# Kernel optimization log

Measured on AMD Instinct MI355X. Metric: run time of the kernel, lower is better.

## Reference

```python
import jax, jax.numpy as jnp
import numpy as np

L, B, S, D, H, F = 4, 8, 512, 512, 8, 2048
KS = (1, 3, 5)
DEPTH = D // H


def causal_conv(x, W, b):
    # x: [B,S,D], W: [k,D,D] (WIO), causal left pad k-1
    k = W.shape[0]
    y = jax.lax.conv_general_dilated(x, W, (1,), [(k - 1, 0)],
                                     dimension_numbers=('NWC', 'WIO', 'NWC'))
    return y + b


def layer_norm(x, g, b, eps=1e-6):
    mu = jnp.mean(x, -1, keepdims=True)
    var = jnp.mean((x - mu) ** 2, -1, keepdims=True)
    return (x - mu) * jax.lax.rsqrt(var + eps) * g + b


def split_heads(t):
    return t.reshape(B, S, H, DEPTH).transpose(0, 2, 1, 3)  # [B,H,S,depth]


def setup_inputs() -> dict:
    key = jax.random.key(0)
    keys = iter(jax.random.split(key, 16))
    rn = lambda shape, s=0.02: jax.random.normal(next(keys), shape, jnp.float32) * s
    inp = {"x": jax.random.normal(next(keys), (B, S, D), jnp.float32)}
    for k in KS:
        inp[f"Wq{k}"] = rn((L, k, D, D))
        inp[f"Wk{k}"] = rn((L, k, D, D))
    inp["bq"] = jnp.zeros((L, 3, D), jnp.float32)
    inp["bk"] = jnp.zeros((L, 3, D), jnp.float32)
    inp["Wv"] = rn((L, 3, 1, D, D))
    inp["bv"] = jnp.zeros((L, 3, D), jnp.float32)
    inp["Wo"] = rn((L, D, D)); inp["bo"] = jnp.zeros((L, D), jnp.float32)
    inp["W1"] = rn((L, D, F)); inp["b1"] = jnp.zeros((L, F), jnp.float32)
    inp["W2"] = rn((L, F, D)); inp["b2"] = jnp.zeros((L, D), jnp.float32)
    inp["ln1_g"] = jnp.ones((L, D), jnp.float32); inp["ln1_b"] = jnp.zeros((L, D), jnp.float32)
    inp["ln2_g"] = jnp.ones((L, D), jnp.float32); inp["ln2_b"] = jnp.zeros((L, D), jnp.float32)
    return inp


def reference(x, Wq1, Wq3, Wq5, Wk1, Wk3, Wk5, bq, bk, Wv, bv, Wo, bo,
              W1, b1, W2, b2, ln1_g, ln1_b, ln2_g, ln2_b):
    # causal look-ahead mask: 1 - band_part(ones, -1, 0), added as mask * -1e9
    neg_mask = (1.0 - jnp.tril(jnp.ones((S, S), jnp.float32))) * -1e9
    scale = 1.0 / jnp.sqrt(jnp.float32(DEPTH))
    Wqs, Wks = (Wq1, Wq3, Wq5), (Wk1, Wk3, Wk5)
    for l in range(L):
        outs = []
        for i in range(len(KS)):
            q = split_heads(causal_conv(x, Wqs[i][l], bq[l, i]))
            k = split_heads(causal_conv(x, Wks[i][l], bk[l, i]))
            v = split_heads(causal_conv(x, Wv[l, i], bv[l, i]))
            logits = jnp.einsum('bhqd,bhkd->bhqk', q, k) * scale + neg_mask
            a = jax.nn.softmax(logits, axis=-1)
            o = jnp.einsum('bhqk,bhkd->bhqd', a, v)
            outs.append(o.transpose(0, 2, 1, 3).reshape(B, S, D))
        attn_out = ((outs[0] + outs[1] + outs[2]) / 3.0) @ Wo[l] + bo[l]
        out1 = layer_norm(attn_out + x, ln1_g[l], ln1_b[l])
        ffn = jax.nn.relu(out1 @ W1[l] + b1[l]) @ W2[l] + b2[l]
        x = layer_norm(ffn + out1, ln2_g[l], ln2_b[l])
    return x
```

## Files before the change

### kernel.cpp

```cpp
#include <hip/hip_runtime.h>
#include <cstdint>
#include <cstddef>

#define Dm 512
#define Sm 512
#define Bm 8
#define Hm 8
#define Fm 2048
#define Mm 4096
#define Lm 4

typedef __bf16 bf16x8 __attribute__((ext_vector_type(8)));
typedef float  fx4    __attribute__((ext_vector_type(4)));
typedef float  fx2    __attribute__((ext_vector_type(2)));
typedef unsigned short u16;
typedef unsigned short u16x4 __attribute__((ext_vector_type(4)));
typedef short s16x8 __attribute__((ext_vector_type(8)));

__device__ __forceinline__ u16 f2b(float f) {
  union { float f; uint32_t u; } v; v.f = f;
  uint32_t u = v.u;
  return (u16)((u + 0x7fffu + ((u >> 16) & 1u)) >> 16);
}
__device__ __forceinline__ float b2f(u16 h) {
  union { uint32_t u; float f; } v; v.u = ((uint32_t)h) << 16;
  return v.f;
}

__device__ __forceinline__ void gload16(const void* g, void* l) {
  __builtin_amdgcn_global_load_lds(
      (const __attribute__((address_space(1))) void*)g,
      (__attribute__((address_space(3))) void*)l, 16, 0, 0);
}

template<int N>
__device__ __forceinline__ void vwait() {
  if constexpr (N == 4)      asm volatile("s_waitcnt vmcnt(4)" ::: "memory");
  else if constexpr (N == 8) asm volatile("s_waitcnt vmcnt(8)" ::: "memory");
  else                       asm volatile("s_waitcnt vmcnt(0)" ::: "memory");
}

__global__ void cast_bf16_kernel(const float* __restrict__ in, u16* __restrict__ out,
                                 u16* __restrict__ zpad) {
  int i = (blockIdx.x * 256 + threadIdx.x) * 4;
  fx4 v = *(const fx4*)(in + i);
  u16x4 o;
  #pragma unroll
  for (int j = 0; j < 4; ++j) o[j] = f2b(v[j]);
  *(u16x4*)(out + i) = o;
  if (blockIdx.x == 0) { zpad[threadIdx.x] = 0; zpad[threadIdx.x + 256] = 0; }
}

__global__ void avg3_kernel(const u16* __restrict__ o3, u16* __restrict__ out) {
  int i = (blockIdx.x * 256 + threadIdx.x) * 4;
  u16x4 a = *(const u16x4*)(o3 + i);
  u16x4 b = *(const u16x4*)(o3 + (size_t)Mm*Dm + i);
  u16x4 c = *(const u16x4*)(o3 + (size_t)2*Mm*Dm + i);
  u16x4 r;
  #pragma unroll
  for (int j = 0; j < 4; ++j)
    r[j] = f2b((b2f(a[j]) + b2f(b[j]) + b2f(c[j])) * (1.f/3.f));
  *(u16x4*)(out + i) = r;
}

__global__ void ln_kernel(const float* __restrict__ in, const float* __restrict__ gam,
                          const float* __restrict__ bet, float* __restrict__ outf,
                          u16* __restrict__ outb) {
  int row = blockIdx.x;
  int t = threadIdx.x;
  const float* x = in + (size_t)row * Dm;
  fx4 v0 = *(const fx4*)(x + t*4);
  fx4 v1 = *(const fx4*)(x + 256 + t*4);
  float s = 0.f, sq = 0.f;
  #pragma unroll
  for (int j = 0; j < 4; ++j) { s += v0[j] + v1[j]; sq += v0[j]*v0[j] + v1[j]*v1[j]; }
  #pragma unroll
  for (int off = 1; off < 64; off <<= 1) { s += __shfl_xor(s, off, 64); sq += __shfl_xor(sq, off, 64); }
  float mu  = s * (1.f/Dm);
  float var = sq * (1.f/Dm) - mu*mu;
  float rstd = rsqrtf(var + 1e-6f);
  fx4 g0 = *(const fx4*)(gam + t*4), g1 = *(const fx4*)(gam + 256 + t*4);
  fx4 b0 = *(const fx4*)(bet + t*4), b1 = *(const fx4*)(bet + 256 + t*4);
  float* of = outf + (size_t)row*Dm;
  u16*   ob = outb + (size_t)row*Dm;
  fx4 y0, y1; u16x4 h0, h1;
  #pragma unroll
  for (int j = 0; j < 4; ++j) {
    y0[j] = (v0[j]-mu)*rstd*g0[j] + b0[j];
    y1[j] = (v1[j]-mu)*rstd*g1[j] + b1[j];
    h0[j] = f2b(y0[j]); h1[j] = f2b(y1[j]);
  }
  *(fx4*)(of + t*4) = y0; *(fx4*)(of + 256 + t*4) = y1;
  *(u16x4*)(ob + t*4) = h0; *(u16x4*)(ob + 256 + t*4) = h1;
}

#define TST 130
__global__ void prep_kernel(u16* __restrict__ packed,
    const float* __restrict__ Wq1, const float* __restrict__ Wq3, const float* __restrict__ Wq5,
    const float* __restrict__ Wk1, const float* __restrict__ Wk3, const float* __restrict__ Wk5,
    const float* __restrict__ Wv,  const float* __restrict__ Wo,
    const float* __restrict__ W1,  const float* __restrict__ W2, int layer) {
  __shared__ float T[64 * TST];
  constexpr int t0[13] = {0,32,128,288,320,416,576,608,640,672,704,832,960};
  int bid = blockIdx.x;
  int seg = 0;
  while (bid >= t0[seg+1]) ++seg;
  int local = bid - t0[seg];
  const float* src; int K, N;
  switch (seg) {
    case 0:  src = Wq1 + (size_t)layer*512*512;   K = 512;  N = 512;  break;
    case 1:  src = Wq3 + (size_t)layer*3*512*512; K = 1536; N = 512;  break;
    case 2:  src = Wq5 + (size_t)layer*5*512*512; K = 2560; N = 512;  break;
    case 3:  src = Wk1 + (size_t)layer*512*512;   K = 512;  N = 512;  break;
    case 4:  src = Wk3 + (size_t)layer*3*512*512; K = 1536; N = 512;  break;
    case 5:  src = Wk5 + (size_t)layer*5*512*512; K = 2560; N = 512;  break;
    case 6:  src = Wv + (size_t)(layer*3+0)*512*512; K = 512; N = 512; break;
    case 7:  src = Wv + (size_t)(layer*3+1)*512*512; K = 512; N = 512; break;
    case 8:  src = Wv + (size_t)(layer*3+2)*512*512; K = 512; N = 512; break;
    case 9:  src = Wo + (size_t)layer*512*512;    K = 512;  N = 512;  break;
    case 10: src = W1 + (size_t)layer*512*2048;   K = 512;  N = 2048; break;
    default: src = W2 + (size_t)layer*2048*512;   K = 2048; N = 512;  break;
  }
  int KT = K >> 6;
  int ntile = local / KT, ktile = local - ntile*KT;
  const float* sb = src + (size_t)(ktile*64)*N + ntile*128;
  int tid = threadIdx.x;
  #pragma unroll
  for (int i = 0; i < 16; ++i) {
    int idx = i*256 + tid;
    int row = idx >> 6, col2 = (idx & 63) * 2;
    fx2 v = *(const fx2*)(sb + (size_t)row*N + col2);
    *(fx2*)(&T[row*TST + col2]) = v;
  }
  __syncthreads();
  u16* dst = packed + ((size_t)bid << 13);
  #pragma unroll
  for (int j = 0; j < 4; ++j) {
    int z = j*256 + tid;
    int row = z >> 3;
    int c = (z & 7) ^ (row & 7);
    s16x8 o;
    #pragma unroll
    for (int e = 0; e < 8; ++e) o[e] = (short)f2b(T[(c*8 + e)*TST + row]);
    *(s16x8*)(dst + z*8) = o;
  }
}

#define GEMM_STEP(IDX, CB, NB, BC, BN, NRv, NW)                                   \
  {                                                                              \
    bool hn = (IDX) + 1 < ntiles;                                                \
    if (hn) {                                                                    \
      stageA(NB);                                                                \
      ++skt; if (skt == KTt) { skt = 0; ++st; }                                  \
      const u16* wtn = WtN + ((size_t)((IDX) + 1) << 13);                        \
      _Pragma("unroll")                                                          \
      for (int kk = 0; kk < 2; ++kk)                                             \
        _Pragma("unroll")                                                        \
        for (int n = 0; n < NRv; ++n) {                                          \
          int row = wn*(NRv*16) + n*16 + r16;                                    \
          BN[kk][n] = *(const bf16x8*)(wtn + (row << 6) + (((kk*4 + g) ^ (row & 7)) << 3)); \
        }                                                                        \
    }                                                                            \
    bf16x8 a_[2][4];                                                             \
    _Pragma("unroll")                                                            \
    for (int kk = 0; kk < 2; ++kk)                                               \
      _Pragma("unroll")                                                          \
      for (int m = 0; m < 4; ++m) {                                              \
        int row = wm*64 + m*16 + r16;                                            \
        a_[kk][m] = *(const bf16x8*)(&As[CB][(row << 6) + (((kk*4 + g) ^ (row & 7)) << 3)]); \
      }                                                                          \
    __builtin_amdgcn_s_setprio(1);                                               \
    _Pragma("unroll")                                                            \
    for (int kk = 0; kk < 2; ++kk)                                               \
      _Pragma("unroll")                                                          \
      for (int m = 0; m < 4; ++m)                                                \
        _Pragma("unroll")                                                        \
        for (int n = 0; n < NRv; ++n)                                            \
          acc[m][n] = __builtin_amdgcn_mfma_f32_16x16x32_bf16(a_[kk][m], BC[kk][n], acc[m][n], 0, 0, 0); \
    __builtin_amdgcn_s_setprio(0);                                               \
    vwait<2*NRv>();                                                              \
    __builtin_amdgcn_s_barrier();                                                \
  }

__global__ __launch_bounds__(256, 2) void conv_all(const u16* __restrict__ xb,
    const u16* __restrict__ packed,
    const float* __restrict__ bq, const float* __restrict__ bk, const float* __restrict__ bv,
    u16* __restrict__ qb, u16* __restrict__ kb, u16* __restrict__ vT, int layer,
    const u16* __restrict__ zpad) {
  __shared__ __align__(16) u16 As[2][8192];
  constexpr int t0c[9]   = {0,32,128,288,320,416,576,608,640};
  constexpr int tapsc[9] = {1,3,5,1,3,5,1,1,1};
  constexpr int order[9] = {2,5,1,4,0,3,6,7,8};
  int bid = blockIdx.x;
  int unit = order[bid >> 7];
  int local = bid & 127;
  int mtile = local >> 2, ntile = local & 3;
  int taps = tapsc[unit];
  int brow = mtile * 128, bcol = ntile * 128;
  int tid = threadIdx.x, lane = tid & 63, wid = tid >> 6;
  int wm = wid >> 1, wn = wid & 1;
  int r16 = lane & 15, g = lane >> 4;
  const u16* WtN = packed + ((size_t)(t0c[unit] + ntile * taps * 8) << 13);
  fx4 acc[4][4] = {};
  int ntiles = taps * 8;
  const int KTt = 8;
  int st = 0, skt = 0;
  auto stageA = [&](int bufi) {
    int shift = taps - 1 - st;
    int c0 = skt << 6;
    #pragma unroll
    for (int j = 0; j < 4; ++j) {
      int zb = wid*256 + j*64;
      int zz = zb + lane;
      int row = zz >> 3, c = (zz & 7) ^ (row & 7);
      int s = (brow + row) & (Sm - 1);
      const u16* src = (s >= shift) ? (xb + (size_t)(brow + row - shift)*Dm + c0 + c*8) : zpad;
      gload16(src, &As[bufi][zb * 8]);
    }
  };
  bf16x8 bA[2][4], bB[2][4];
  stageA(0);
  ++skt; if (skt == KTt) { skt = 0; ++st; }
  #pragma unroll
  for (int kk = 0; kk < 2; ++kk)
    #pragma unroll
    for (int n = 0; n < 4; ++n) {
      int row = wn*64 + n*16 + r16;
      bA[kk][n] = *(const bf16x8*)(WtN + (row << 6) + (((kk*4 + g) ^ (row & 7)) << 3));
    }
  __syncthreads();
  for (int base = 0; base < ntiles; base += 2) {
    GEMM_STEP(base,     0, 1, bA, bB, 4, 2)
    GEMM_STEP(base + 1, 1, 0, bB, bA, 4, 2)
  }
  const float* bias; u16* outp;
  if (unit < 3)      { bias = bq + (size_t)(layer*3 + unit)*Dm;   outp = qb + (size_t)unit*Mm*Dm; }
  else if (unit < 6) { bias = bk + (size_t)(layer*3 + unit-3)*Dm; outp = kb + (size_t)(unit-3)*Mm*Dm; }
  else               { bias = bv + (size_t)(layer*3 + unit-6)*Dm; outp = vT + ((size_t)(unit-6) << 21); }
  if (unit < 6) {
    #pragma unroll
    for (int m = 0; m < 4; ++m) {
      int row0 = brow + wm*64 + m*16 + g*4;
      #pragma unroll
      for (int n = 0; n < 4; ++n) {
        int col = bcol + wn*64 + n*16 + r16;
        float bv_ = bias[col];
        #pragma unroll
        for (int r = 0; r < 4; ++r)
          outp[(size_t)(row0 + r)*Dm + col] = f2b(acc[m][n][r] + bv_);
      }
    }
  } else {
    #pragma unroll
    for (int m = 0; m < 4; ++m) {
      int row0 = brow + wm*64 + m*16 + g*4;
      int bidx = row0 >> 9, spos = row0 & 511;
      #pragma unroll
      for (int n = 0; n < 4; ++n) {
        int col = bcol + wn*64 + n*16 + r16;
        int hh = col >> 6, dd = col & 63;
        float bv_ = bias[col];
        u16x4 pk;
        #pragma unroll
        for (int r = 0; r < 4; ++r) pk[r] = f2b(acc[m][n][r] + bv_);
        *(u16x4*)(outp + (((size_t)(bidx*8 + hh)*64 + dd) << 9) + spos) = pk;
      }
    }
  }
}

template<int MODE, int BMt, int WN, bool CAUSAL>
__device__ __forceinline__ void gemm_core(const u16* __restrict__ A, int lda, int Ktap, int taps,
    const u16* __restrict__ Wt, const float* __restrict__ bias, const float* __restrict__ res,
    u16* __restrict__ outb, float* __restrict__ outf, int N, const u16* __restrict__ zpad) {
  constexpr int NR = 128 / (16 * WN);
  constexpr int AD = BMt / 32;
  __shared__ __align__(16) u16 As[2][BMt * 64];
  int tid = threadIdx.x, lane = tid & 63, wid = tid >> 6;
  int wm = (WN == 2) ? (wid >> 1) : 0;
  int wn = (WN == 2) ? (wid & 1) : wid;
  int r16 = lane & 15, g = lane >> 4;
  int brow = blockIdx.x * BMt, bcol = blockIdx.y * 128;
  const int KTt = Ktap >> 6;
  const u16* WtN = Wt + ((size_t)(blockIdx.y * taps * KTt) << 13);
  fx4 acc[4][NR] = {};
  int ntiles = taps * KTt;
  int st = 0, skt = 0;
  auto stageA = [&](int bufi) {
    int shift = taps - 1 - st;
    int c0 = skt << 6;
    #pragma unroll
    for (int j = 0; j < AD; ++j) {
      int zb = wid*(BMt*2) + j*64;
      int zz = zb + lane;
      int row = zz >> 3, c = (zz & 7) ^ (row & 7);
      const u16* src;
      if (CAUSAL) {
        int s = (brow + row) & (Sm - 1);
        src = (s >= shift) ? (A + (size_t)(brow + row - shift)*lda + c0 + c*8) : zpad;
      } else {
        src = A + (size_t)(brow + row)*lda + c0 + c*8;
      }
      gload16(src, &As[bufi][zb * 8]);
    }
  };
  bf16x8 bA[2][NR], bB[2][NR];
  stageA(0);
  ++skt; if (skt == KTt) { skt = 0; ++st; }
  #pragma unroll
  for (int kk = 0; kk < 2; ++kk)
    #pragma unroll
    for (int n = 0; n < NR; ++n) {
      int row = wn*(NR*16) + n*16 + r16;
      bA[kk][n] = *(const bf16x8*)(WtN + (row << 6) + (((kk*4 + g) ^ (row & 7)) << 3));
    }
  __syncthreads();
  for (int base = 0; base < ntiles; base += 2) {
    GEMM_STEP(base,     0, 1, bA, bB, NR, WN)
    GEMM_STEP(base + 1, 1, 0, bB, bA, NR, WN)
  }
  #pragma unroll
  for (int m = 0; m < 4; ++m) {
    int row0 = brow + wm*64 + m*16 + g*4;
    #pragma unroll
    for (int n = 0; n < NR; ++n) {
      int col = bcol + wn*(NR*16) + n*16 + r16;
      float bv_ = bias[col];
      #pragma unroll
      for (int r = 0; r < 4; ++r) {
        size_t idx = (size_t)(row0 + r)*N + col;
        float v = acc[m][n][r] + bv_;
        if (MODE == 0)      outb[idx] = f2b(v);
        else if (MODE == 1) outb[idx] = f2b(fmaxf(v, 0.f));
        else                outf[idx] = v + res[idx];
      }
    }
  }
}

template<int MODE, int BMt, int WN, int LB>
__global__ __launch_bounds__(256, LB) void gemm_dense(const u16* __restrict__ A, int lda, int K,
    const u16* __restrict__ Wt, const float* __restrict__ bias, const float* __restrict__ res,
    u16* __restrict__ outb, float* __restrict__ outf, int N) {
  gemm_core<MODE, BMt, WN, false>(A, lda, K, 1, Wt, bias, res, outb, outf, N, nullptr);
}

__global__ __launch_bounds__(256, 3) void attn_kernel(const u16* __restrict__ qb,
    const u16* __restrict__ kb, const u16* __restrict__ vTb, u16* __restrict__ ob) {
  __shared__ __align__(16) u16 Ks[2][4096];
  __shared__ __align__(16) u16 Vs[2][4096];
  __shared__ __align__(16) u16 Ps[4][1024];
  int a = blockIdx.x, bh = blockIdx.y, br = blockIdx.z;
  int b = bh >> 3, h = bh & 7;
  const u16* q  = qb + (size_t)br*Mm*Dm;
  const u16* k  = kb + (size_t)br*Mm*Dm;
  const u16* vT = vTb + (((size_t)br << 21) + ((size_t)bh << 15));
  u16* o = ob + (size_t)br*Mm*Dm;
  int tid = threadIdx.x, lane = tid & 63, wid = tid >> 6;
  int r16 = lane & 15, g = lane >> 4;
  size_t rowbase = (size_t)b * Sm;
  int qt[2] = {7 - a, a};
  int nkt = qt[0] + 1;

  bf16x8 qa[2][2];
  #pragma unroll
  for (int t2 = 0; t2 < 2; ++t2)
    #pragma unroll
    for (int c = 0; c < 2; ++c)
      qa[t2][c] = *(const bf16x8*)(q + (rowbase + qt[t2]*64 + wid*16 + r16)*Dm + h*64 + c*32 + g*8);

  float m_[2][4], l_[2][4];
  fx4 accO[2][4] = {};
  #pragma unroll
  for (int t2 = 0; t2 < 2; ++t2)
    #pragma unroll
    for (int r = 0; r < 4; ++r) { m_[t2][r] = -3.0e38f; l_[t2][r] = 0.f; }

  auto stage = [&](int kt, int bufi) {
    #pragma unroll
    for (int it = 0; it < 2; ++it) {
      int zb = wid*128 + it*64;
      int zz = zb + lane;
      int row = zz >> 3, c = (zz & 7) ^ (row & 7);
      gload16(k + (rowbase + kt*64 + row)*Dm + h*64 + c*8, &Ks[bufi][zb * 8]);
      gload16(vT + ((size_t)row << 9) + kt*64 + c*8, &Vs[bufi][zb * 8]);
    }
  };
  stage(0, 0);
  __syncthreads();

  for (int kt = 0; kt < nkt; ++kt) {
    int cur = kt & 1;
    if (kt + 1 < nkt) stage(kt + 1, cur ^ 1);
    #pragma unroll
    for (int t2 = 0; t2 < 2; ++t2) {
      if (t2 == 0 || kt <= qt[1]) {
        fx4 sacc[4] = {};
        #pragma unroll
        for (int c = 0; c < 2; ++c)
          #pragma unroll
          for (int n = 0; n < 4; ++n) {
            int row = n*16 + r16;
            bf16x8 kf = *(const bf16x8*)(&Ks[cur][(row << 6) + (((c*4 + g) ^ (row & 7)) << 3)]);
            sacc[n] = __builtin_amdgcn_mfma_f32_16x16x32_bf16(qa[t2][c], kf, sacc[n], 0, 0, 0);
          }
        float sv[4][4];
        bool diag = (kt == qt[t2]);
        #pragma unroll
        for (int n = 0; n < 4; ++n)
          #pragma unroll
          for (int r = 0; r < 4; ++r) {
            float s = sacc[n][r] * 0.125f;
            if (diag && (n*16 + r16 > wid*16 + g*4 + r)) s = -3.0e38f;
            sv[n][r] = s;
          }
        #pragma unroll
        for (int r = 0; r < 4; ++r) {
          float rm = fmaxf(fmaxf(sv[0][r], sv[1][r]), fmaxf(sv[2][r], sv[3][r]));
          #pragma unroll
          for (int off = 1; off < 16; off <<= 1) rm = fmaxf(rm, __shfl_xor(rm, off, 64));
          float mnew = fmaxf(m_[t2][r], rm);
          float corr = __expf(m_[t2][r] - mnew);
          m_[t2][r] = mnew;
          float rs = 0.f;
          #pragma unroll
          for (int n = 0; n < 4; ++n) { float p = __expf(sv[n][r] - mnew); sv[n][r] = p; rs += p; }
          #pragma unroll
          for (int off = 1; off < 16; off <<= 1) rs += __shfl_xor(rs, off, 64);
          l_[t2][r] = l_[t2][r]*corr + rs;
          #pragma unroll
          for (int n = 0; n < 4; ++n) accO[t2][n][r] *= corr;
        }
        #pragma unroll
        for (int n = 0; n < 4; ++n)
          #pragma unroll
          for (int r = 0; r < 4; ++r) {
            int qq = g*4 + r;
            Ps[wid][(qq << 6) + (((n*2 + (r16 >> 3)) ^ (qq & 7)) << 3) + (r16 & 7)] = f2b(sv[n][r]);
          }
        #pragma unroll
        for (int kk = 0; kk < 2; ++kk) {
          bf16x8 pa = *(const bf16x8*)(&Ps[wid][(r16 << 6) + (((kk*4 + g) ^ (r16 & 7)) << 3)]);
          #pragma unroll
          for (int n = 0; n < 4; ++n) {
            int row = n*16 + r16;
            bf16x8 vf = *(const bf16x8*)(&Vs[cur][(row << 6) + (((kk*4 + g) ^ (row & 7)) << 3)]);
            accO[t2][n] = __builtin_amdgcn_mfma_f32_16x16x32_bf16(pa, vf, accO[t2][n], 0, 0, 0);
          }
        }
      }
    }
    __syncthreads();
  }
  #pragma unroll
  for (int t2 = 0; t2 < 2; ++t2)
    #pragma unroll
    for (int n = 0; n < 4; ++n)
      #pragma unroll
      for (int r = 0; r < 4; ++r) {
        int qrow = qt[t2]*64 + wid*16 + g*4 + r;
        o[(rowbase + qrow)*Dm + h*64 + n*16 + r16] = f2b(accO[t2][n][r] / l_[t2][r]);
      }
}

extern "C" void kernel_launch(void* const* d_in, const int* in_sizes, int n_in,
                              void* d_out, int out_size, void* d_ws, size_t ws_size,
                              hipStream_t stream) {
  const float* x_in = (const float*)d_in[0];
  const float* Wq1 = (const float*)d_in[1];
  const float* Wk1 = (const float*)d_in[2];
  const float* Wq3 = (const float*)d_in[3];
  const float* Wk3 = (const float*)d_in[4];
  const float* Wq5 = (const float*)d_in[5];
  const float* Wk5 = (const float*)d_in[6];
  const float* bq  = (const float*)d_in[7];
  const float* bk  = (const float*)d_in[8];
  const float* Wv  = (const float*)d_in[9];
  const float* bv  = (const float*)d_in[10];
  const float* Wo  = (const float*)d_in[11];
  const float* bo  = (const float*)d_in[12];
  const float* W1  = (const float*)d_in[13];
  const float* b1  = (const float*)d_in[14];
  const float* W2  = (const float*)d_in[15];
  const float* b2  = (const float*)d_in[16];
  const float* ln1g = (const float*)d_in[17];
  const float* ln1b = (const float*)d_in[18];
  const float* ln2g = (const float*)d_in[19];
  const float* ln2b = (const float*)d_in[20];

  char* ws = (char*)d_ws;
  size_t off = 0;
  auto alloc = [&](size_t bytes) { void* p = ws + off; off += (bytes + 255) & ~(size_t)255; return p; };
  float* x_f32 = (float*)alloc((size_t)Mm*Dm*4);
  u16*   xb    = (u16*)  alloc((size_t)Mm*Dm*2);
  u16*   qbuf  = (u16*)  alloc((size_t)3*Mm*Dm*2);
  u16*   kbuf  = (u16*)  alloc((size_t)3*Mm*Dm*2);
  u16*   vT    = (u16*)  alloc((size_t)3*Mm*Dm*2);
  u16*   obuf  = (u16*)  alloc((size_t)3*Mm*Dm*2);
  u16*   avgb  = (u16*)  alloc((size_t)Mm*Dm*2);
  float* pre   = (float*)alloc((size_t)Mm*Dm*4);
  float* out1f = (float*)alloc((size_t)Mm*Dm*4);
  u16*   out1b = (u16*)  alloc((size_t)Mm*Dm*2);
  u16*   midb  = (u16*)  alloc((size_t)Mm*Fm*2);
  u16*   packed= (u16*)  alloc((size_t)960*8192*2);
  u16*   zpad  = (u16*)  alloc(1024);

  cast_bf16_kernel<<<2048, 256, 0, stream>>>(x_in, xb, zpad);
  for (int l = 0; l < Lm; ++l) {
    const float* xs = (l == 0) ? x_in : x_f32;
    prep_kernel<<<960, 256, 0, stream>>>(packed, Wq1, Wq3, Wq5, Wk1, Wk3, Wk5,
                                         Wv, Wo, W1, W2, l);
    conv_all<<<1152, 256, 0, stream>>>(
        xb, packed, bq, bk, bv, qbuf, kbuf, vT, l, zpad);
    attn_kernel<<<dim3(4, 64, 3), 256, 0, stream>>>(qbuf, kbuf, vT, obuf);
    avg3_kernel<<<2048, 256, 0, stream>>>(obuf, avgb);
    gemm_dense<2, 64, 4, 3><<<dim3(64, 4), 256, 0, stream>>>(
        avgb, 512, 512, packed + ((size_t)672 << 13), bo + (size_t)l*Dm, xs, nullptr, pre, 512);
    ln_kernel<<<4096, 64, 0, stream>>>(pre, ln1g + (size_t)l*Dm, ln1b + (size_t)l*Dm, out1f, out1b);
    gemm_dense<1, 128, 2, 2><<<dim3(32, 16), 256, 0, stream>>>(
        out1b, 512, 512, packed + ((size_t)704 << 13), b1 + (size_t)l*Fm, nullptr, midb, nullptr, 2048);
    gemm_dense<2, 64, 4, 3><<<dim3(64, 4), 256, 0, stream>>>(
        midb, 2048, 2048, packed + ((size_t)832 << 13), b2 + (size_t)l*Dm, out1f, nullptr, pre, 512);
    float* lnout = (l == Lm-1) ? (float*)d_out : x_f32;
    ln_kernel<<<4096, 64, 0, stream>>>(pre, ln2g + (size_t)l*Dm, ln2b + (size_t)l*Dm, lnout, xb);
  }
}
```

Baseline: 620.4 us.

## Restructure GEMM main loop with per-half-K waits and full-width warp tiles

```diff
diff --git a/kernel.cpp b/kernel.cpp
--- a/kernel.cpp
+++ b/kernel.cpp
@@ -35,9 +35,10 @@
 
 template<int N>
 __device__ __forceinline__ void vwait() {
-  if constexpr (N == 4)      asm volatile("s_waitcnt vmcnt(4)" ::: "memory");
-  else if constexpr (N == 8) asm volatile("s_waitcnt vmcnt(8)" ::: "memory");
-  else                       asm volatile("s_waitcnt vmcnt(0)" ::: "memory");
+  if constexpr (N == 8)       asm volatile("s_waitcnt vmcnt(8)"  ::: "memory");
+  else if constexpr (N == 12) asm volatile("s_waitcnt vmcnt(12)" ::: "memory");
+  else if constexpr (N == 20) asm volatile("s_waitcnt vmcnt(20)" ::: "memory");
+  else                        asm volatile("s_waitcnt vmcnt(0)"  ::: "memory");
 }
 
 __global__ void cast_bf16_kernel(const float* __restrict__ in, u16* __restrict__ out,
@@ -66,8 +67,8 @@
 __global__ void ln_kernel(const float* __restrict__ in, const float* __restrict__ gam,
                           const float* __restrict__ bet, float* __restrict__ outf,
                           u16* __restrict__ outb) {
-  int row = blockIdx.x;
-  int t = threadIdx.x;
+  int row = blockIdx.x * 4 + (threadIdx.x >> 6);
+  int t = threadIdx.x & 63;
   const float* x = in + (size_t)row * Dm;
   fx4 v0 = *(const fx4*)(x + t*4);
   fx4 v1 = *(const fx4*)(x + 256 + t*4);
@@ -146,40 +147,52 @@
   }
 }
 
-#define GEMM_STEP(IDX, CB, NB, BC, BN, NRv, NW)                                   \
-  {                                                                              \
-    bool hn = (IDX) + 1 < ntiles;                                                \
-    if (hn) {                                                                    \
-      stageA(NB);                                                                \
-      ++skt; if (skt == KTt) { skt = 0; ++st; }                                  \
-      const u16* wtn = WtN + ((size_t)((IDX) + 1) << 13);                        \
-      _Pragma("unroll")                                                          \
-      for (int kk = 0; kk < 2; ++kk)                                             \
-        _Pragma("unroll")                                                        \
-        for (int n = 0; n < NRv; ++n) {                                          \
-          int row = wn*(NRv*16) + n*16 + r16;                                    \
-          BN[kk][n] = *(const bf16x8*)(wtn + (row << 6) + (((kk*4 + g) ^ (row & 7)) << 3)); \
-        }                                                                        \
-    }                                                                            \
-    bf16x8 a_[2][4];                                                             \
-    _Pragma("unroll")                                                            \
-    for (int kk = 0; kk < 2; ++kk)                                               \
-      _Pragma("unroll")                                                          \
-      for (int m = 0; m < 4; ++m) {                                              \
-        int row = wm*64 + m*16 + r16;                                            \
-        a_[kk][m] = *(const bf16x8*)(&As[CB][(row << 6) + (((kk*4 + g) ^ (row & 7)) << 3)]); \
-      }                                                                          \
-    __builtin_amdgcn_s_setprio(1);                                               \
-    _Pragma("unroll")                                                            \
-    for (int kk = 0; kk < 2; ++kk)                                               \
-      _Pragma("unroll")                                                          \
-      for (int m = 0; m < 4; ++m)                                                \
-        _Pragma("unroll")                                                        \
-        for (int n = 0; n < NRv; ++n)                                            \
-          acc[m][n] = __builtin_amdgcn_mfma_f32_16x16x32_bf16(a_[kk][m], BC[kk][n], acc[m][n], 0, 0, 0); \
-    __builtin_amdgcn_s_setprio(0);                                               \
-    vwait<2*NRv>();                                                              \
-    __builtin_amdgcn_s_barrier();                                                \
+#define KSTEP(IDX, CB, BC, BN)                                                    \
+  {                                                                               \
+    bool hn = (IDX) + 1 < ntiles;                                                 \
+    const u16* wtc = WtN + ((size_t)(IDX) << 13);                                 \
+    bf16x8 bH[8];                                                                 \
+    _Pragma("unroll")                                                             \
+    for (int n = 0; n < 8; ++n) {                                                 \
+      int row = n*16 + r16;                                                       \
+      bH[n] = *(const bf16x8*)(wtc + (row << 6) + (((4 + g) ^ (row & 7)) << 3));  \
+    }                                                                             \
+    if (hn) {                                                                     \
+      stageA((CB) ^ 1);                                                           \
+      ++skt; if (skt == KTt) { skt = 0; ++st; }                                   \
+      const u16* wtn = WtN + ((size_t)((IDX) + 1) << 13);                         \
+      _Pragma("unroll")                                                           \
+      for (int n = 0; n < 8; ++n) {                                               \
+        int row = n*16 + r16;                                                     \
+        BN[n] = *(const bf16x8*)(wtn + (row << 6) + (((g) ^ (row & 7)) << 3));    \
+      }                                                                           \
+      vwait<20>();                                                                \
+    } else {                                                                      \
+      vwait<8>();                                                                 \
+    }                                                                             \
+    bf16x8 a0[MR];                                                                \
+    _Pragma("unroll")                                                             \
+    for (int m = 0; m < MR; ++m) {                                                \
+      int row = wrow + m*16 + r16;                                                \
+      a0[m] = *(const bf16x8*)(&As[CB][(row << 6) + (((g) ^ (row & 7)) << 3)]);   \
+    }                                                                             \
+    _Pragma("unroll")                                                             \
+    for (int m = 0; m < MR; ++m)                                                  \
+      _Pragma("unroll")                                                           \
+      for (int n = 0; n < 8; ++n)                                                 \
+        acc[m][n] = __builtin_amdgcn_mfma_f32_16x16x32_bf16(a0[m], BC[n], acc[m][n], 0, 0, 0); \
+    if (hn) vwait<12>(); else vwait<0>();                                         \
+    bf16x8 a1[MR];                                                                \
+    _Pragma("unroll")                                                             \
+    for (int m = 0; m < MR; ++m) {                                                \
+      int row = wrow + m*16 + r16;                                                \
+      a1[m] = *(const bf16x8*)(&As[CB][(row << 6) + (((4 + g) ^ (row & 7)) << 3)]); \
+    }                                                                             \
+    _Pragma("unroll")                                                             \
+    for (int m = 0; m < MR; ++m)                                                  \
+      _Pragma("unroll")                                                           \
+      for (int n = 0; n < 8; ++n)                                                 \
+        acc[m][n] = __builtin_amdgcn_mfma_f32_16x16x32_bf16(a1[m], bH[n], acc[m][n], 0, 0, 0); \
   }
 
 __global__ __launch_bounds__(256, 2) void conv_all(const u16* __restrict__ xb,
@@ -187,6 +200,7 @@
     const float* __restrict__ bq, const float* __restrict__ bk, const float* __restrict__ bv,
     u16* __restrict__ qb, u16* __restrict__ kb, u16* __restrict__ vT, int layer,
     const u16* __restrict__ zpad) {
+  constexpr int MR = 2;
   __shared__ __align__(16) u16 As[2][8192];
   constexpr int t0c[9]   = {0,32,128,288,320,416,576,608,640};
   constexpr int tapsc[9] = {1,3,5,1,3,5,1,1,1};
@@ -198,10 +212,10 @@
   int taps = tapsc[unit];
   int brow = mtile * 128, bcol = ntile * 128;
   int tid = threadIdx.x, lane = tid & 63, wid = tid >> 6;
-  int wm = wid >> 1, wn = wid & 1;
   int r16 = lane & 15, g = lane >> 4;
+  int wrow = wid * 32;
   const u16* WtN = packed + ((size_t)(t0c[unit] + ntile * taps * 8) << 13);
-  fx4 acc[4][4] = {};
+  fx4 acc[MR][8] = {};
   int ntiles = taps * 8;
   const int KTt = 8;
   int st = 0, skt = 0;
@@ -218,20 +232,17 @@
       gload16(src, &As[bufi][zb * 8]);
     }
   };
-  bf16x8 bA[2][4], bB[2][4];
+  bf16x8 bC[8], bN[8];
   stageA(0);
   ++skt; if (skt == KTt) { skt = 0; ++st; }
   #pragma unroll
-  for (int kk = 0; kk < 2; ++kk)
-    #pragma unroll
-    for (int n = 0; n < 4; ++n) {
-      int row = wn*64 + n*16 + r16;
-      bA[kk][n] = *(const bf16x8*)(WtN + (row << 6) + (((kk*4 + g) ^ (row & 7)) << 3));
-    }
-  __syncthreads();
+  for (int n = 0; n < 8; ++n) {
+    int row = n*16 + r16;
+    bC[n] = *(const bf16x8*)(WtN + (row << 6) + (((g) ^ (row & 7)) << 3));
+  }
   for (int base = 0; base < ntiles; base += 2) {
-    GEMM_STEP(base,     0, 1, bA, bB, 4, 2)
-    GEMM_STEP(base + 1, 1, 0, bB, bA, 4, 2)
+    KSTEP(base,     0, bC, bN)
+    KSTEP(base + 1, 1, bN, bC)
   }
   const float* bias; u16* outp;
   if (unit < 3)      { bias = bq + (size_t)(layer*3 + unit)*Dm;   outp = qb + (size_t)unit*Mm*Dm; }
@@ -239,11 +250,11 @@
   else               { bias = bv + (size_t)(layer*3 + unit-6)*Dm; outp = vT + ((size_t)(unit-6) << 21); }
   if (unit < 6) {
     #pragma unroll
-    for (int m = 0; m < 4; ++m) {
-      int row0 = brow + wm*64 + m*16 + g*4;
+    for (int m = 0; m < MR; ++m) {
+      int row0 = brow + wrow + m*16 + g*4;
       #pragma unroll
-      for (int n = 0; n < 4; ++n) {
-        int col = bcol + wn*64 + n*16 + r16;
+      for (int n = 0; n < 8; ++n) {
+        int col = bcol + n*16 + r16;
         float bv_ = bias[col];
         #pragma unroll
         for (int r = 0; r < 4; ++r)
@@ -252,12 +263,12 @@
     }
   } else {
     #pragma unroll
-    for (int m = 0; m < 4; ++m) {
-      int row0 = brow + wm*64 + m*16 + g*4;
+    for (int m = 0; m < MR; ++m) {
+      int row0 = brow + wrow + m*16 + g*4;
       int bidx = row0 >> 9, spos = row0 & 511;
       #pragma unroll
-      for (int n = 0; n < 4; ++n) {
-        int col = bcol + wn*64 + n*16 + r16;
+      for (int n = 0; n < 8; ++n) {
+        int col = bcol + n*16 + r16;
         int hh = col >> 6, dd = col & 63;
         float bv_ = bias[col];
         u16x4 pk;
@@ -269,62 +280,51 @@
   }
 }
 
-template<int MODE, int BMt, int WN, bool CAUSAL>
-__device__ __forceinline__ void gemm_core(const u16* __restrict__ A, int lda, int Ktap, int taps,
+template<int MODE, int BMt>
+__device__ __forceinline__ void gemm_core(const u16* __restrict__ A, int lda, int Ktap,
     const u16* __restrict__ Wt, const float* __restrict__ bias, const float* __restrict__ res,
-    u16* __restrict__ outb, float* __restrict__ outf, int N, const u16* __restrict__ zpad) {
-  constexpr int NR = 128 / (16 * WN);
+    u16* __restrict__ outb, float* __restrict__ outf, int N) {
+  constexpr int MR = BMt / 64;
   constexpr int AD = BMt / 32;
   __shared__ __align__(16) u16 As[2][BMt * 64];
   int tid = threadIdx.x, lane = tid & 63, wid = tid >> 6;
-  int wm = (WN == 2) ? (wid >> 1) : 0;
-  int wn = (WN == 2) ? (wid & 1) : wid;
   int r16 = lane & 15, g = lane >> 4;
+  int wrow = wid * (16 * MR);
   int brow = blockIdx.x * BMt, bcol = blockIdx.y * 128;
   const int KTt = Ktap >> 6;
-  const u16* WtN = Wt + ((size_t)(blockIdx.y * taps * KTt) << 13);
-  fx4 acc[4][NR] = {};
-  int ntiles = taps * KTt;
+  const u16* WtN = Wt + ((size_t)(blockIdx.y * KTt) << 13);
+  fx4 acc[MR][8] = {};
+  int ntiles = KTt;
   int st = 0, skt = 0;
+  (void)st;
   auto stageA = [&](int bufi) {
-    int shift = taps - 1 - st;
     int c0 = skt << 6;
     #pragma unroll
     for (int j = 0; j < AD; ++j) {
       int zb = wid*(BMt*2) + j*64;
       int zz = zb + lane;
       int row = zz >> 3, c = (zz & 7) ^ (row & 7);
-      const u16* src;
-      if (CAUSAL) {
-        int s = (brow + row) & (Sm - 1);
-        src = (s >= shift) ? (A + (size_t)(brow + row - shift)*lda + c0 + c*8) : zpad;
-      } else {
-        src = A + (size_t)(brow + row)*lda + c0 + c*8;
-      }
-      gload16(src, &As[bufi][zb * 8]);
+      gload16(A + (size_t)(brow + row)*lda + c0 + c*8, &As[bufi][zb * 8]);
     }
   };
-  bf16x8 bA[2][NR], bB[2][NR];
+  bf16x8 bC[8], bN[8];
   stageA(0);
-  ++skt; if (skt == KTt) { skt = 0; ++st; }
-  #pragma unroll
-  for (int kk = 0; kk < 2; ++kk)
-    #pragma unroll
-    for (int n = 0; n < NR; ++n) {
-      int row = wn*(NR*16) + n*16 + r16;
-      bA[kk][n] = *(const bf16x8*)(WtN + (row << 6) + (((kk*4 + g) ^ (row & 7)) << 3));
-    }
-  __syncthreads();
+  ++skt;
+  #pragma unroll
+  for (int n = 0; n < 8; ++n) {
+    int row = n*16 + r16;
+    bC[n] = *(const bf16x8*)(WtN + (row << 6) + (((g) ^ (row & 7)) << 3));
+  }
   for (int base = 0; base < ntiles; base += 2) {
-    GEMM_STEP(base,     0, 1, bA, bB, NR, WN)
-    GEMM_STEP(base + 1, 1, 0, bB, bA, NR, WN)
-  }
-  #pragma unroll
-  for (int m = 0; m < 4; ++m) {
-    int row0 = brow + wm*64 + m*16 + g*4;
-    #pragma unroll
-    for (int n = 0; n < NR; ++n) {
-      int col = bcol + wn*(NR*16) + n*16 + r16;
+    KSTEP(base,     0, bC, bN)
+    KSTEP(base + 1, 1, bN, bC)
+  }
+  #pragma unroll
+  for (int m = 0; m < MR; ++m) {
+    int row0 = brow + wrow + m*16 + g*4;
+    #pragma unroll
+    for (int n = 0; n < 8; ++n) {
+      int col = bcol + n*16 + r16;
       float bv_ = bias[col];
       #pragma unroll
       for (int r = 0; r < 4; ++r) {
@@ -338,11 +338,11 @@
   }
 }
 
-template<int MODE, int BMt, int WN, int LB>
-__global__ __launch_bounds__(256, LB) void gemm_dense(const u16* __restrict__ A, int lda, int K,
+template<int MODE, int BMt>
+__global__ __launch_bounds__(256, 2) void gemm_dense(const u16* __restrict__ A, int lda, int K,
     const u16* __restrict__ Wt, const float* __restrict__ bias, const float* __restrict__ res,
     u16* __restrict__ outb, float* __restrict__ outf, int N) {
-  gemm_core<MODE, BMt, WN, false>(A, lda, K, 1, Wt, bias, res, outb, outf, N, nullptr);
+  gemm_core<MODE, BMt>(A, lda, K, Wt, bias, res, outb, outf, N);
 }
 
 __global__ __launch_bounds__(256, 3) void attn_kernel(const u16* __restrict__ qb,
@@ -514,14 +514,14 @@
         xb, packed, bq, bk, bv, qbuf, kbuf, vT, l, zpad);
     attn_kernel<<<dim3(4, 64, 3), 256, 0, stream>>>(qbuf, kbuf, vT, obuf);
     avg3_kernel<<<2048, 256, 0, stream>>>(obuf, avgb);
-    gemm_dense<2, 64, 4, 3><<<dim3(64, 4), 256, 0, stream>>>(
+    gemm_dense<2, 64><<<dim3(64, 4), 256, 0, stream>>>(
         avgb, 512, 512, packed + ((size_t)672 << 13), bo + (size_t)l*Dm, xs, nullptr, pre, 512);
-    ln_kernel<<<4096, 64, 0, stream>>>(pre, ln1g + (size_t)l*Dm, ln1b + (size_t)l*Dm, out1f, out1b);
-    gemm_dense<1, 128, 2, 2><<<dim3(32, 16), 256, 0, stream>>>(
+    ln_kernel<<<1024, 256, 0, stream>>>(pre, ln1g + (size_t)l*Dm, ln1b + (size_t)l*Dm, out1f, out1b);
+    gemm_dense<1, 128><<<dim3(32, 16), 256, 0, stream>>>(
         out1b, 512, 512, packed + ((size_t)704 << 13), b1 + (size_t)l*Fm, nullptr, midb, nullptr, 2048);
-    gemm_dense<2, 64, 4, 3><<<dim3(64, 4), 256, 0, stream>>>(
+    gemm_dense<2, 64><<<dim3(64, 4), 256, 0, stream>>>(
         midb, 2048, 2048, packed + ((size_t)832 << 13), b2 + (size_t)l*Dm, out1f, nullptr, pre, 512);
     float* lnout = (l == Lm-1) ? (float*)d_out : x_f32;
-    ln_kernel<<<4096, 64, 0, stream>>>(pre, ln2g + (size_t)l*Dm, ln2b + (size_t)l*Dm, lnout, xb);
-  }
-}
+    ln_kernel<<<1024, 256, 0, stream>>>(pre, ln2g + (size_t)l*Dm, ln2b + (size_t)l*Dm, lnout, xb);
+  }
+}
```

Result: slower. 782.0 us (+26.0%).
